# Kernel tuning notes

Measured on AMD Instinct MI355X. Metric: run time of the kernel, lower is better.

The kernel has to match this reference:

```python
import jax, jax.numpy as jnp
import numpy as np

DIM = 128
N_ITER = 8
L_SIZE = 80000
C_SIZE = 120000
N_EDGES = 480000


def _mlp(x, w1, b1, w2, b2):
    # 2-layer MLP with ReLU (satbench_n_mlp_layers=2, activation='relu')
    return jnp.maximum(x @ w1 + b1, 0.0) @ w2 + b2


def _layer_norm(x, g, b, eps=1e-5):
    mu = jnp.mean(x, axis=-1, keepdims=True)
    var = jnp.var(x, axis=-1, keepdims=True)
    return (x - mu) * jax.lax.rsqrt(var + eps) * g + b


def _ln_lstm_cell(x, h, c, wi, wh, g_ih, b_ih, g_hh, b_hh, g_c, b_c):
    # LayerNormBasicLSTMCell: LN on input/hidden gate pre-activations and on new cell state
    gates = _layer_norm(x @ wi, g_ih, b_ih) + _layer_norm(h @ wh, g_hh, b_hh)
    i, f, g, o = jnp.split(gates, 4, axis=1)
    new_c = jax.nn.sigmoid(f) * c + jax.nn.sigmoid(i) * jnp.tanh(g)
    new_h = jax.nn.sigmoid(o) * jnp.tanh(_layer_norm(new_c, g_c, b_c))
    return new_h, new_c


def setup_inputs() -> dict:
    key = jax.random.key(0)
    ks = jax.random.split(key, 24)
    d = DIM
    s1 = 1.0 / np.sqrt(d)
    s2 = 1.0 / np.sqrt(2 * d)
    inp = {
        'l_size': L_SIZE,
        'c_size': C_SIZE,
        'l_edge_index': jax.random.randint(ks[0], (N_EDGES,), 0, L_SIZE),
        'c_edge_index': jax.random.randint(ks[1], (N_EDGES,), 0, C_SIZE),
        'l_emb': jax.random.normal(ks[2], (L_SIZE, d), jnp.float32),
        'c_emb': jax.random.normal(ks[3], (C_SIZE, d), jnp.float32),
        # l2c message MLP
        'l2c_w1': jax.random.normal(ks[4], (d, d), jnp.float32) * s1,
        'l2c_b1': jnp.zeros((d,), jnp.float32),
        'l2c_w2': jax.random.normal(ks[5], (d, d), jnp.float32) * s1,
        'l2c_b2': jnp.zeros((d,), jnp.float32),
        # c2l message MLP
        'c2l_w1': jax.random.normal(ks[6], (d, d), jnp.float32) * s1,
        'c2l_b1': jnp.zeros((d,), jnp.float32),
        'c2l_w2': jax.random.normal(ks[7], (d, d), jnp.float32) * s1,
        'c2l_b2': jnp.zeros((d,), jnp.float32),
        # clause update LSTM (input=d)
        'cu_wi': jax.random.normal(ks[8], (d, 4 * d), jnp.float32) * s1,
        'cu_wh': jax.random.normal(ks[9], (d, 4 * d), jnp.float32) * s1,
        'cu_g_ih': jnp.ones((4 * d,), jnp.float32),
        'cu_b_ih': jnp.zeros((4 * d,), jnp.float32),
        'cu_g_hh': jnp.ones((4 * d,), jnp.float32),
        'cu_b_hh': jnp.zeros((4 * d,), jnp.float32),
        'cu_g_c': jnp.ones((d,), jnp.float32),
        'cu_b_c': jnp.zeros((d,), jnp.float32),
        # literal update LSTM (input=2*d)
        'lu_wi': jax.random.normal(ks[10], (2 * d, 4 * d), jnp.float32) * s2,
        'lu_wh': jax.random.normal(ks[11], (d, 4 * d), jnp.float32) * s1,
        'lu_g_ih': jnp.ones((4 * d,), jnp.float32),
        'lu_b_ih': jnp.zeros((4 * d,), jnp.float32),
        'lu_g_hh': jnp.ones((4 * d,), jnp.float32),
        'lu_b_hh': jnp.zeros((4 * d,), jnp.float32),
        'lu_g_c': jnp.ones((d,), jnp.float32),
        'lu_b_c': jnp.zeros((d,), jnp.float32),
    }
    return inp


def reference(l_size, c_size, l_edge_index, c_edge_index, l_emb, c_emb,
              l2c_w1, l2c_b1, l2c_w2, l2c_b2,
              c2l_w1, c2l_b1, c2l_w2, c2l_b2,
              cu_wi, cu_wh, cu_g_ih, cu_b_ih, cu_g_hh, cu_b_hh, cu_g_c, cu_b_c,
              lu_wi, lu_wh, lu_g_ih, lu_b_ih, lu_g_hh, lu_b_hh, lu_g_c, lu_b_c):
    d = l_emb.shape[1]
    l_state = jnp.zeros((l_size, d), l_emb.dtype)
    c_state = jnp.zeros((c_size, d), c_emb.dtype)
    l_embs = [l_emb]
    c_embs = [c_emb]
    for _ in range(N_ITER):
        # literal -> clause
        l_msg_feat = _mlp(l_emb, l2c_w1, l2c_b1, l2c_w2, l2c_b2)
        l2c_msg = l_msg_feat[l_edge_index]                             # [E, d] gather
        l2c_aggr = jax.ops.segment_sum(l2c_msg, c_edge_index, num_segments=c_size)
        c_emb, c_state = _ln_lstm_cell(l2c_aggr, c_emb, c_state,
                                       cu_wi, cu_wh, cu_g_ih, cu_b_ih,
                                       cu_g_hh, cu_b_hh, cu_g_c, cu_b_c)
        c_embs.append(c_emb)
        # clause -> literal
        c_msg_feat = _mlp(c_emb, c2l_w1, c2l_b1, c2l_w2, c2l_b2)
        c2l_msg = c_msg_feat[c_edge_index]
        c2l_aggr = jax.ops.segment_sum(c2l_msg, l_edge_index, num_segments=l_size)
        # flip pos/neg literal embeddings (l2l message)
        pl, ul = jnp.split(l_emb.reshape(l_size // 2, 2 * d), 2, axis=1)
        l2l_msg = jnp.concatenate([ul, pl], axis=1).reshape(l_size, d)
        l_emb, l_state = _ln_lstm_cell(jnp.concatenate([c2l_aggr, l2l_msg], axis=1),
                                       l_emb, l_state,
                                       lu_wi, lu_wh, lu_g_ih, lu_b_ih,
                                       lu_g_hh, lu_b_hh, lu_g_c, lu_b_c)
        l_embs.append(l_emb)
    return jnp.stack(l_embs), jnp.stack(c_embs)
```

## Files before the change

kernel.cpp:

```cpp
#include <hip/hip_runtime.h>
#include <hip/hip_bf16.h>

#define L_SIZE 80000
#define C_SIZE 120000
#define N_EDGES 480000
#define DIM 128
#define GDIM 512
#define N_ITER 8
#define MAXDEG 64

typedef __attribute__((ext_vector_type(8))) short short8;
typedef __attribute__((ext_vector_type(4))) float f32x4;

__device__ __forceinline__ ushort f2bf(float f) {
    uint u = __float_as_uint(f);
    u = u + 0x7FFFu + ((u >> 16) & 1u);
    return (ushort)(u >> 16);
}
__device__ __forceinline__ float bf2f(ushort h) {
    return __uint_as_float(((uint)h) << 16);
}
__device__ __forceinline__ void split2(float f, short& hi, short& lo) {
    uint u = __float_as_uint(f);
    hi = (short)(u >> 16);
    float r = f - __uint_as_float(u & 0xFFFF0000u);
    lo = (short)(__float_as_uint(r) >> 16);
}
__device__ __forceinline__ float sigmf(float x) { return 1.f / (1.f + __expf(-x)); }
__device__ __forceinline__ float tanh_f(float x) {
    float e = __expf(2.f * x);
    return 1.f - 2.f / (e + 1.f);
}
__device__ __forceinline__ f32x4 fzero4() {
    f32x4 v; v[0] = v[1] = v[2] = v[3] = 0.f; return v;
}

__global__ __launch_bounds__(256) void fill_ell(
    const int* __restrict__ src, const int* __restrict__ dst,
    int* __restrict__ cnt, int* __restrict__ ell)
{
    int i = blockIdx.x * 256 + threadIdx.x;
    int d = dst[i];
    int pos = atomicAdd(&cnt[d], 1);
    ell[(size_t)d * MAXDEG + pos] = src[i];
}

__global__ __launch_bounds__(256) void pack_w2(const float* __restrict__ W,
                                               ushort* __restrict__ Ph,
                                               ushort* __restrict__ Pl, int K, int N)
{
    int NC = N / 16;
    int total = K * N;
    for (int o = blockIdx.x * 256 + threadIdx.x; o < total; o += gridDim.x * 256) {
        int j = o & 7, hi = (o >> 3) & 3, c = (o >> 5) & 15;
        int rest = o >> 9;
        int cc = rest % NC, ks = rest / NC;
        int row = ks * 32 + hi * 8 + j, col = cc * 16 + c;
        float v = W[(size_t)row * N + col];
        ushort h = f2bf(v);
        Ph[o] = h;
        Pl[o] = f2bf(v - bf2f(h));
    }
}

__device__ __forceinline__ void stageA2(const float* __restrict__ src, int rowBase,
                                        ushort* dst, int tid, int nrows)
{
    const int planeB = nrows * 256;
    for (int idx = tid * 8; idx < nrows * 128; idx += 512 * 8) {
        int r = idx >> 7, k8 = idx & 127;
        const float* p = src + (size_t)(rowBase + r) * DIM + k8;
        float4 v0 = *(const float4*)p;
        float4 v1 = *(const float4*)(p + 4);
        float f[8] = {v0.x, v0.y, v0.z, v0.w, v1.x, v1.y, v1.z, v1.w};
        short8 hi8, lo8;
        #pragma unroll
        for (int j = 0; j < 8; ++j) {
            short h, l;
            split2(f[j], h, l);
            hi8[j] = h;
            lo8[j] = l;
        }
        int boff = r * 256 + ((k8 * 2) ^ ((r & 7) << 4));
        *(short8*)((char*)dst + boff) = hi8;
        *(short8*)((char*)dst + planeB + boff) = lo8;
    }
}

__device__ __forceinline__ short8 readA(const ushort* As, int mi, int k0, int lane)
{
    int r = mi * 16 + (lane & 15);
    int kb = (k0 * 2 + ((lane >> 4) << 4)) ^ ((r & 7) << 4);
    return *(const short8*)((const char*)As + r * 256 + kb);
}

__device__ __forceinline__ short8 readAf(const ushort* As, int mi, int k0, int lane)
{
    int r = (mi * 16 + (lane & 15)) ^ 1;
    int kb = (k0 * 2 + ((lane >> 4) << 4)) ^ ((r & 7) << 4);
    return *(const short8*)((const char*)As + r * 256 + kb);
}

__device__ __forceinline__ short8 readB(const ushort* P, int ks, int NC, int cc,
                                        int laneOff)
{
    return *(const short8*)((const char*)P + (((size_t)(ks * NC + cc)) << 10) + laneOff);
}

#define MFMA3(acc, ah, al, bh, bl)                                              \
    acc = __builtin_amdgcn_mfma_f32_16x16x32_bf16(ah, bh, acc, 0, 0, 0);        \
    acc = __builtin_amdgcn_mfma_f32_16x16x32_bf16(ah, bl, acc, 0, 0, 0);        \
    acc = __builtin_amdgcn_mfma_f32_16x16x32_bf16(al, bh, acc, 0, 0, 0);

__global__ __launch_bounds__(512, 4) void mlp_kernel(
    const float* __restrict__ A,
    const ushort* __restrict__ w1Ph, const ushort* __restrict__ w1Pl,
    const float* __restrict__ b1,
    const ushort* __restrict__ w2Ph, const ushort* __restrict__ w2Pl,
    const float* __restrict__ b2,
    float* __restrict__ msg)
{
    __shared__ __align__(16) ushort AsIn[2 * 64 * 128];
    __shared__ __align__(16) ushort AsHid[2 * 64 * 128];
    const int tid = threadIdx.x;
    const int wv = tid >> 6, lane = tid & 63;
    const int cl = lane & 15, hi = lane >> 4;
    const int rowBase = blockIdx.x * 64;
    const int laneOff = (cl * 4 + hi) * 16;
    const int col = wv * 16 + cl;

    stageA2(A, rowBase, AsIn, tid, 64);
    float b1c = b1[col], b2c = b2[col];
    __syncthreads();

    f32x4 acc[4];
    #pragma unroll
    for (int mi = 0; mi < 4; ++mi) acc[mi] = fzero4();
    #pragma unroll
    for (int ks = 0; ks < 4; ++ks) {
        short8 bh = readB(w1Ph, ks, 8, wv, laneOff);
        short8 bl = readB(w1Pl, ks, 8, wv, laneOff);
        #pragma unroll
        for (int mi = 0; mi < 4; ++mi) {
            short8 ah = readA(AsIn, mi, ks * 32, lane);
            short8 al = readA(AsIn + 64 * 128, mi, ks * 32, lane);
            MFMA3(acc[mi], ah, al, bh, bl);
        }
    }
    #pragma unroll
    for (int mi = 0; mi < 4; ++mi)
        #pragma unroll
        for (int q = 0; q < 4; ++q) {
            int row = mi * 16 + hi * 4 + q;
            float v = fmaxf(acc[mi][q] + b1c, 0.f);
            short h2, l2;
            split2(v, h2, l2);
            int boff = row * 256 + ((2 * col) ^ ((row & 7) << 4));
            *(short*)((char*)AsHid + boff) = h2;
            *(short*)((char*)AsHid + 64 * 256 + boff) = l2;
        }
    __syncthreads();

    f32x4 acc2[4];
    #pragma unroll
    for (int mi = 0; mi < 4; ++mi) acc2[mi] = fzero4();
    #pragma unroll
    for (int ks = 0; ks < 4; ++ks) {
        short8 bh = readB(w2Ph, ks, 8, wv, laneOff);
        short8 bl = readB(w2Pl, ks, 8, wv, laneOff);
        #pragma unroll
        for (int mi = 0; mi < 4; ++mi) {
            short8 ah = readA(AsHid, mi, ks * 32, lane);
            short8 al = readA(AsHid + 64 * 128, mi, ks * 32, lane);
            MFMA3(acc2[mi], ah, al, bh, bl);
        }
    }
    #pragma unroll
    for (int mi = 0; mi < 4; ++mi)
        #pragma unroll
        for (int q = 0; q < 4; ++q) {
            int row = mi * 16 + hi * 4 + q;
            msg[(size_t)(rowBase + row) * DIM + col] = acc2[mi][q] + b2c;
        }
}

template<int KX>
__global__ __launch_bounds__(512, 4) void lstm_kernel(
    const float* __restrict__ msg, const int* __restrict__ cnt,
    const int* __restrict__ ell,
    const float* __restrict__ Hsrc,
    const ushort* __restrict__ wiPh, const ushort* __restrict__ wiPl,
    const ushort* __restrict__ whPh, const ushort* __restrict__ whPl,
    const float* __restrict__ g_ih, const float* __restrict__ b_ih,
    const float* __restrict__ g_hh, const float* __restrict__ b_hh,
    const float* __restrict__ g_c,  const float* __restrict__ b_c,
    float* __restrict__ c_state, float* __restrict__ h_out)
{
    __shared__ __align__(16) ushort AsX0[2 * 32 * 128];
    __shared__ __align__(16) ushort AsH [2 * 32 * 128];
    __shared__ float Cs[32][132];
    __shared__ float red4f[32 * 33];
    __shared__ float lnstf[32 * 4];
    __shared__ float red2f[32 * 17];
    __shared__ float lncf[32 * 2];

    const int tid = threadIdx.x;
    const int wv = tid >> 6, lane = tid & 63;
    const int cl = lane & 15, hi = lane >> 4;
    const int rowBase = blockIdx.x * 32;
    const int laneOff = (cl * 4 + hi) * 16;
    const int d = wv * 16 + cl;

    stageA2(Hsrc, rowBase, AsH, tid, 32);
    {
        #pragma unroll
        for (int idx = tid * 4; idx < 32 * 128; idx += 512 * 4) {
            int r = idx >> 7, c = idx & 127;
            *(float4*)&Cs[r][c] =
                *(const float4*)(c_state + (size_t)(rowBase + r) * DIM + c);
        }
    }

    {
        int r = tid >> 4;
        int d8 = (tid & 15) << 3;
        int row = rowBase + r;
        int deg = cnt[row];
        const int* sl = ell + (size_t)row * MAXDEG;
        float a0=0,a1=0,a2=0,a3=0,a4=0,a5=0,a6=0,a7=0;
        for (int k = 0; k < deg; k += 4) {
            int i0 = sl[k], i1 = sl[k+1], i2 = sl[k+2], i3 = sl[k+3];
            const float* m0 = msg + (size_t)i0 * DIM + d8;
            const float* m1 = msg + (size_t)i1 * DIM + d8;
            const float* m2 = msg + (size_t)i2 * DIM + d8;
            const float* m3 = msg + (size_t)i3 * DIM + d8;
            float4 p00 = *(const float4*)m0,       p01 = *(const float4*)(m0 + 4);
            float4 p10 = *(const float4*)m1,       p11 = *(const float4*)(m1 + 4);
            float4 p20 = *(const float4*)m2,       p21 = *(const float4*)(m2 + 4);
            float4 p30 = *(const float4*)m3,       p31 = *(const float4*)(m3 + 4);
            float w1 = (k + 1 < deg) ? 1.f : 0.f;
            float w2 = (k + 2 < deg) ? 1.f : 0.f;
            float w3 = (k + 3 < deg) ? 1.f : 0.f;
            a0 += p00.x; a1 += p00.y; a2 += p00.z; a3 += p00.w;
            a4 += p01.x; a5 += p01.y; a6 += p01.z; a7 += p01.w;
            a0 += w1 * p10.x; a1 += w1 * p10.y; a2 += w1 * p10.z; a3 += w1 * p10.w;
            a4 += w1 * p11.x; a5 += w1 * p11.y; a6 += w1 * p11.z; a7 += w1 * p11.w;
            a0 += w2 * p20.x; a1 += w2 * p20.y; a2 += w2 * p20.z; a3 += w2 * p20.w;
            a4 += w2 * p21.x; a5 += w2 * p21.y; a6 += w2 * p21.z; a7 += w2 * p21.w;
            a0 += w3 * p30.x; a1 += w3 * p30.y; a2 += w3 * p30.z; a3 += w3 * p30.w;
            a4 += w3 * p31.x; a5 += w3 * p31.y; a6 += w3 * p31.z; a7 += w3 * p31.w;
        }
        float f[8] = {a0,a1,a2,a3,a4,a5,a6,a7};
        short8 hi8, lo8;
        #pragma unroll
        for (int j = 0; j < 8; ++j) {
            short h, l;
            split2(f[j], h, l);
            hi8[j] = h;
            lo8[j] = l;
        }
        int boff = r * 256 + ((d8 * 2) ^ ((r & 7) << 4));
        *(short8*)((char*)AsX0 + boff) = hi8;
        *(short8*)((char*)AsX0 + 32 * 256 + boff) = lo8;
    }

    float gih[4], bih[4], ghh[4], bhh[4];
    #pragma unroll
    for (int jb = 0; jb < 4; ++jb) {
        int col = jb * 128 + d;
        gih[jb] = g_ih[col]; bih[jb] = b_ih[col];
        ghh[jb] = g_hh[col]; bhh[jb] = b_hh[col];
    }
    const float gcv = g_c[d], bcv = b_c[d];
    __syncthreads();

    f32x4 xacc[2][4], hacc[2][4];
    #pragma unroll
    for (int mi = 0; mi < 2; ++mi)
        #pragma unroll
        for (int jb = 0; jb < 4; ++jb) { xacc[mi][jb] = fzero4(); hacc[mi][jb] = fzero4(); }

    #pragma unroll
    for (int ks = 0; ks < KX; ++ks) {
        int k0 = (ks & 3) * 32;
        short8 axh0, axl0, axh1, axl1;
        if (KX == 8 && ks >= 4) {
            axh0 = readAf(AsH, 0, k0, lane);
            axl0 = readAf(AsH + 32 * 128, 0, k0, lane);
            axh1 = readAf(AsH, 1, k0, lane);
            axl1 = readAf(AsH + 32 * 128, 1, k0, lane);
        } else {
            axh0 = readA(AsX0, 0, k0, lane);
            axl0 = readA(AsX0 + 32 * 128, 0, k0, lane);
            axh1 = readA(AsX0, 1, k0, lane);
            axl1 = readA(AsX0 + 32 * 128, 1, k0, lane);
        }
        #pragma unroll
        for (int jb = 0; jb < 4; ++jb) {
            short8 bh = readB(wiPh, ks, 32, jb * 8 + wv, laneOff);
            short8 bl = readB(wiPl, ks, 32, jb * 8 + wv, laneOff);
            MFMA3(xacc[0][jb], axh0, axl0, bh, bl);
            MFMA3(xacc[1][jb], axh1, axl1, bh, bl);
        }
        if (ks < 4) {
            short8 ahh0 = readA(AsH, 0, k0, lane);
            short8 ahl0 = readA(AsH + 32 * 128, 0, k0, lane);
            short8 ahh1 = readA(AsH, 1, k0, lane);
            short8 ahl1 = readA(AsH + 32 * 128, 1, k0, lane);
            #pragma unroll
            for (int jb = 0; jb < 4; ++jb) {
                short8 bh = readB(whPh, ks, 32, jb * 8 + wv, laneOff);
                short8 bl = readB(whPl, ks, 32, jb * 8 + wv, laneOff);
                MFMA3(hacc[0][jb], ahh0, ahl0, bh, bl);
                MFMA3(hacc[1][jb], ahh1, ahl1, bh, bl);
            }
        }
    }

    #pragma unroll
    for (int mi = 0; mi < 2; ++mi)
        #pragma unroll
        for (int q = 0; q < 4; ++q) {
            float px = 0.f, pqx = 0.f, ph = 0.f, pqh = 0.f;
            #pragma unroll
            for (int jb = 0; jb < 4; ++jb) {
                float v = xacc[mi][jb][q]; px += v; pqx += v * v;
                float u = hacc[mi][jb][q]; ph += u; pqh += u * u;
            }
            #pragma unroll
            for (int m = 1; m < 16; m <<= 1) {
                px += __shfl_xor(px, m); pqx += __shfl_xor(pqx, m);
                ph += __shfl_xor(ph, m); pqh += __shfl_xor(pqh, m);
            }
            if (cl == 0) {
                int row = mi * 16 + hi * 4 + q;
                float* rp = red4f + row * 33 + wv * 4;
                rp[0] = px; rp[1] = pqx; rp[2] = ph; rp[3] = pqh;
            }
        }
    __syncthreads();
    if (tid < 32) {
        float sx = 0.f, qx = 0.f, sh = 0.f, qh = 0.f;
        const float* rp = red4f + tid * 33;
        for (int ww = 0; ww < 8; ++ww) {
            sx += rp[ww * 4 + 0]; qx += rp[ww * 4 + 1];
            sh += rp[ww * 4 + 2]; qh += rp[ww * 4 + 3];
        }
        const float inv = 1.f / 512.f;
        float mux = sx * inv, muh = sh * inv;
        lnstf[tid * 4 + 0] = mux;
        lnstf[tid * 4 + 1] = rsqrtf(qx * inv - mux * mux + 1e-5f);
        lnstf[tid * 4 + 2] = muh;
        lnstf[tid * 4 + 3] = rsqrtf(qh * inv - muh * muh + 1e-5f);
    }
    __syncthreads();

    float cn[2][4], og[2][4];
    #pragma unroll
    for (int mi = 0; mi < 2; ++mi)
        #pragma unroll
        for (int q = 0; q < 4; ++q) {
            int row = mi * 16 + hi * 4 + q;
            float mux = lnstf[row * 4 + 0], rx = lnstf[row * 4 + 1];
            float muh = lnstf[row * 4 + 2], rh = lnstf[row * 4 + 3];
            float g4[4];
            #pragma unroll
            for (int jb = 0; jb < 4; ++jb)
                g4[jb] = (xacc[mi][jb][q] - mux) * rx * gih[jb] + bih[jb]
                       + (hacc[mi][jb][q] - muh) * rh * ghh[jb] + bhh[jb];
            float cp = Cs[row][d];
            float cv = sigmf(g4[1]) * cp + sigmf(g4[0]) * tanh_f(g4[2]);
            cn[mi][q] = cv; og[mi][q] = g4[3];
            float sc = cv, qc = cv * cv;
            #pragma unroll
            for (int m = 1; m < 16; m <<= 1) {
                sc += __shfl_xor(sc, m); qc += __shfl_xor(qc, m);
            }
            if (cl == 0) {
                float* rp = red2f + row * 17 + wv * 2;
                rp[0] = sc; rp[1] = qc;
            }
        }
    __syncthreads();
    if (tid < 32) {
        float sc = 0.f, qc = 0.f;
        const float* rp = red2f + tid * 17;
        for (int ww = 0; ww < 8; ++ww) { sc += rp[ww * 2]; qc += rp[ww * 2 + 1]; }
        const float inv = 1.f / 128.f;
        float mu = sc * inv;
        lncf[tid * 2 + 0] = mu;
        lncf[tid * 2 + 1] = rsqrtf(qc * inv - mu * mu + 1e-5f);
    }
    __syncthreads();

    #pragma unroll
    for (int mi = 0; mi < 2; ++mi)
        #pragma unroll
        for (int q = 0; q < 4; ++q) {
            int row = mi * 16 + hi * 4 + q;
            size_t go = (size_t)(rowBase + row) * DIM + d;
            float cv = cn[mi][q];
            float hv = sigmf(og[mi][q]) *
                       tanh_f((cv - lncf[row * 2]) * lncf[row * 2 + 1] * gcv + bcv);
            c_state[go] = cv;
            h_out[go] = hv;
        }
}

extern "C" void kernel_launch(void* const* d_in, const int* in_sizes, int n_in,
                              void* d_out, int out_size, void* d_ws, size_t ws_size,
                              hipStream_t stream)
{
    const int*   l_edge  = (const int*)d_in[2];
    const int*   c_edge  = (const int*)d_in[3];
    const float* l_emb0  = (const float*)d_in[4];
    const float* c_emb0  = (const float*)d_in[5];
    const float* l2c_w1  = (const float*)d_in[6];
    const float* l2c_b1  = (const float*)d_in[7];
    const float* l2c_w2  = (const float*)d_in[8];
    const float* l2c_b2  = (const float*)d_in[9];
    const float* c2l_w1  = (const float*)d_in[10];
    const float* c2l_b1  = (const float*)d_in[11];
    const float* c2l_w2  = (const float*)d_in[12];
    const float* c2l_b2  = (const float*)d_in[13];
    const float* cu_wi   = (const float*)d_in[14];
    const float* cu_wh   = (const float*)d_in[15];
    const float* cu_g_ih = (const float*)d_in[16];
    const float* cu_b_ih = (const float*)d_in[17];
    const float* cu_g_hh = (const float*)d_in[18];
    const float* cu_b_hh = (const float*)d_in[19];
    const float* cu_g_c  = (const float*)d_in[20];
    const float* cu_b_c  = (const float*)d_in[21];
    const float* lu_wi   = (const float*)d_in[22];
    const float* lu_wh   = (const float*)d_in[23];
    const float* lu_g_ih = (const float*)d_in[24];
    const float* lu_b_ih = (const float*)d_in[25];
    const float* lu_g_hh = (const float*)d_in[26];
    const float* lu_b_hh = (const float*)d_in[27];
    const float* lu_g_c  = (const float*)d_in[28];
    const float* lu_b_c  = (const float*)d_in[29];

    float* out = (float*)d_out;
    float* l_slab = out;
    float* c_slab = out + (size_t)9 * L_SIZE * DIM;

    char* wp = (char*)d_ws;
    float*  l_state = (float*)wp;  wp += (size_t)L_SIZE * DIM * 4;
    float*  c_state = (float*)wp;  wp += (size_t)C_SIZE * DIM * 4;
    float*  msg     = (float*)wp;  wp += (size_t)C_SIZE * DIM * 4;
    int* c_cnt = (int*)wp; wp += C_SIZE * 4;
    int* l_cnt = (int*)wp; wp += L_SIZE * 4;
    int* c_ell = (int*)wp; wp += (size_t)C_SIZE * MAXDEG * 4;
    int* l_ell = (int*)wp; wp += (size_t)L_SIZE * MAXDEG * 4;
    ushort* l2c_w1Ph = (ushort*)wp; wp += 128 * 128 * 2;
    ushort* l2c_w1Pl = (ushort*)wp; wp += 128 * 128 * 2;
    ushort* l2c_w2Ph = (ushort*)wp; wp += 128 * 128 * 2;
    ushort* l2c_w2Pl = (ushort*)wp; wp += 128 * 128 * 2;
    ushort* c2l_w1Ph = (ushort*)wp; wp += 128 * 128 * 2;
    ushort* c2l_w1Pl = (ushort*)wp; wp += 128 * 128 * 2;
    ushort* c2l_w2Ph = (ushort*)wp; wp += 128 * 128 * 2;
    ushort* c2l_w2Pl = (ushort*)wp; wp += 128 * 128 * 2;
    ushort* cu_wiPh  = (ushort*)wp; wp += 128 * 512 * 2;
    ushort* cu_wiPl  = (ushort*)wp; wp += 128 * 512 * 2;
    ushort* cu_whPh  = (ushort*)wp; wp += 128 * 512 * 2;
    ushort* cu_whPl  = (ushort*)wp; wp += 128 * 512 * 2;
    ushort* lu_wiPh  = (ushort*)wp; wp += 256 * 512 * 2;
    ushort* lu_wiPl  = (ushort*)wp; wp += 256 * 512 * 2;
    ushort* lu_whPh  = (ushort*)wp; wp += 128 * 512 * 2;
    ushort* lu_whPl  = (ushort*)wp; wp += 128 * 512 * 2;

    const int eb = N_EDGES / 256;

    hipMemsetAsync(c_cnt, 0, C_SIZE * 4, stream);
    hipMemsetAsync(l_cnt, 0, L_SIZE * 4, stream);
    hipMemsetAsync(c_ell, 0, (size_t)C_SIZE * MAXDEG * 4, stream);
    hipMemsetAsync(l_ell, 0, (size_t)L_SIZE * MAXDEG * 4, stream);
    fill_ell<<<eb, 256, 0, stream>>>(l_edge, c_edge, c_cnt, c_ell);
    fill_ell<<<eb, 256, 0, stream>>>(c_edge, l_edge, l_cnt, l_ell);

    pack_w2<<<64, 256, 0, stream>>>(l2c_w1, l2c_w1Ph, l2c_w1Pl, 128, 128);
    pack_w2<<<64, 256, 0, stream>>>(l2c_w2, l2c_w2Ph, l2c_w2Pl, 128, 128);
    pack_w2<<<64, 256, 0, stream>>>(c2l_w1, c2l_w1Ph, c2l_w1Pl, 128, 128);
    pack_w2<<<64, 256, 0, stream>>>(c2l_w2, c2l_w2Ph, c2l_w2Pl, 128, 128);
    pack_w2<<<256, 256, 0, stream>>>(cu_wi, cu_wiPh, cu_wiPl, 128, 512);
    pack_w2<<<256, 256, 0, stream>>>(cu_wh, cu_whPh, cu_whPl, 128, 512);
    pack_w2<<<512, 256, 0, stream>>>(lu_wi, lu_wiPh, lu_wiPl, 256, 512);
    pack_w2<<<256, 256, 0, stream>>>(lu_wh, lu_whPh, lu_whPl, 128, 512);

    hipMemcpyAsync(l_slab, l_emb0, (size_t)L_SIZE * DIM * sizeof(float),
                   hipMemcpyDeviceToDevice, stream);
    hipMemcpyAsync(c_slab, c_emb0, (size_t)C_SIZE * DIM * sizeof(float),
                   hipMemcpyDeviceToDevice, stream);
    hipMemsetAsync(l_state, 0, (size_t)L_SIZE * DIM * sizeof(float), stream);
    hipMemsetAsync(c_state, 0, (size_t)C_SIZE * DIM * sizeof(float), stream);

    for (int t = 0; t < N_ITER; ++t) {
        const float* le = l_slab + (size_t)t * L_SIZE * DIM;
        const float* ce = c_slab + (size_t)t * C_SIZE * DIM;
        float* le1 = l_slab + (size_t)(t + 1) * L_SIZE * DIM;
        float* ce1 = c_slab + (size_t)(t + 1) * C_SIZE * DIM;

        mlp_kernel<<<L_SIZE / 64, 512, 0, stream>>>(le, l2c_w1Ph, l2c_w1Pl, l2c_b1,
                                                    l2c_w2Ph, l2c_w2Pl, l2c_b2, msg);
        lstm_kernel<4><<<C_SIZE / 32, 512, 0, stream>>>(
            msg, c_cnt, c_ell, ce,
            cu_wiPh, cu_wiPl, cu_whPh, cu_whPl,
            cu_g_ih, cu_b_ih, cu_g_hh, cu_b_hh, cu_g_c, cu_b_c,
            c_state, ce1);

        mlp_kernel<<<C_SIZE / 64, 512, 0, stream>>>(ce1, c2l_w1Ph, c2l_w1Pl, c2l_b1,
                                                    c2l_w2Ph, c2l_w2Pl, c2l_b2, msg);
        lstm_kernel<8><<<L_SIZE / 32, 512, 0, stream>>>(
            msg, l_cnt, l_ell, le,
            lu_wiPh, lu_wiPl, lu_whPh, lu_whPl,
            lu_g_ih, lu_b_ih, lu_g_hh, lu_b_hh, lu_g_c, lu_b_c,
            l_state, le1);
    }
}
```

Measured before the change: 5.372 ms.

## Fuse message MLPs into LSTM epilogues and stage messages in output slab

Each LSTM kernel now runs the next stage's 2-layer message MLP on its freshly computed hidden rows. It splits them into bf16 hi/lo in shared memory and writes the messages directly, which removes both standalone MLP launches per iteration and the re-read of embeddings from global memory. The literal-to-clause messages are placed in the next output slab slot, which is overwritten only after the clause LSTM has consumed them, so one MLP launch before the loop seeds the first iteration. The shared-memory staging of the previous cell state is also dropped in favour of direct global reads, which lowers LDS use. In exchange, each LSTM block takes on extra MFMA work and two more barriers.

```diff
diff --git a/kernel.cpp b/kernel.cpp
--- a/kernel.cpp
+++ b/kernel.cpp
@@ -194,11 +194,15 @@
     const float* __restrict__ g_ih, const float* __restrict__ b_ih,
     const float* __restrict__ g_hh, const float* __restrict__ b_hh,
     const float* __restrict__ g_c,  const float* __restrict__ b_c,
-    float* __restrict__ c_state, float* __restrict__ h_out)
+    float* __restrict__ c_state, float* __restrict__ h_out,
+    const ushort* __restrict__ m1Ph, const ushort* __restrict__ m1Pl,
+    const float* __restrict__ mb1,
+    const ushort* __restrict__ m2Ph, const ushort* __restrict__ m2Pl,
+    const float* __restrict__ mb2,
+    float* __restrict__ msg_out)
 {
     __shared__ __align__(16) ushort AsX0[2 * 32 * 128];
     __shared__ __align__(16) ushort AsH [2 * 32 * 128];
-    __shared__ float Cs[32][132];
     __shared__ float red4f[32 * 33];
     __shared__ float lnstf[32 * 4];
     __shared__ float red2f[32 * 17];
@@ -212,14 +216,6 @@
     const int d = wv * 16 + cl;
 
     stageA2(Hsrc, rowBase, AsH, tid, 32);
-    {
-        #pragma unroll
-        for (int idx = tid * 4; idx < 32 * 128; idx += 512 * 4) {
-            int r = idx >> 7, c = idx & 127;
-            *(float4*)&Cs[r][c] =
-                *(const float4*)(c_state + (size_t)(rowBase + r) * DIM + c);
-        }
-    }
 
     {
         int r = tid >> 4;
@@ -368,7 +364,7 @@
             for (int jb = 0; jb < 4; ++jb)
                 g4[jb] = (xacc[mi][jb][q] - mux) * rx * gih[jb] + bih[jb]
                        + (hacc[mi][jb][q] - muh) * rh * ghh[jb] + bhh[jb];
-            float cp = Cs[row][d];
+            float cp = c_state[(size_t)(rowBase + row) * DIM + d];
             float cv = sigmf(g4[1]) * cp + sigmf(g4[0]) * tanh_f(g4[2]);
             cn[mi][q] = cv; og[mi][q] = g4[3];
             float sc = cv, qc = cv * cv;
@@ -404,7 +400,65 @@
                        tanh_f((cv - lncf[row * 2]) * lncf[row * 2 + 1] * gcv + bcv);
             c_state[go] = cv;
             h_out[go] = hv;
-        }
+            if (msg_out) {
+                short h2, l2;
+                split2(hv, h2, l2);
+                int boff = row * 256 + ((2 * d) ^ ((row & 7) << 4));
+                *(short*)((char*)AsX0 + boff) = h2;
+                *(short*)((char*)AsX0 + 32 * 256 + boff) = l2;
+            }
+        }
+
+    if (msg_out) {
+        float mb1c = mb1[d], mb2c = mb2[d];
+        __syncthreads();
+        f32x4 macc[2];
+        macc[0] = fzero4(); macc[1] = fzero4();
+        #pragma unroll
+        for (int ks = 0; ks < 4; ++ks) {
+            short8 bh = readB(m1Ph, ks, 8, wv, laneOff);
+            short8 bl = readB(m1Pl, ks, 8, wv, laneOff);
+            #pragma unroll
+            for (int mi = 0; mi < 2; ++mi) {
+                short8 ah = readA(AsX0, mi, ks * 32, lane);
+                short8 al = readA(AsX0 + 32 * 128, mi, ks * 32, lane);
+                MFMA3(macc[mi], ah, al, bh, bl);
+            }
+        }
+        #pragma unroll
+        for (int mi = 0; mi < 2; ++mi)
+            #pragma unroll
+            for (int q = 0; q < 4; ++q) {
+                int row = mi * 16 + hi * 4 + q;
+                float v = fmaxf(macc[mi][q] + mb1c, 0.f);
+                short h2, l2;
+                split2(v, h2, l2);
+                int boff = row * 256 + ((2 * d) ^ ((row & 7) << 4));
+                *(short*)((char*)AsH + boff) = h2;
+                *(short*)((char*)AsH + 32 * 256 + boff) = l2;
+            }
+        __syncthreads();
+        f32x4 macc2[2];
+        macc2[0] = fzero4(); macc2[1] = fzero4();
+        #pragma unroll
+        for (int ks = 0; ks < 4; ++ks) {
+            short8 bh = readB(m2Ph, ks, 8, wv, laneOff);
+            short8 bl = readB(m2Pl, ks, 8, wv, laneOff);
+            #pragma unroll
+            for (int mi = 0; mi < 2; ++mi) {
+                short8 ah = readA(AsH, mi, ks * 32, lane);
+                short8 al = readA(AsH + 32 * 128, mi, ks * 32, lane);
+                MFMA3(macc2[mi], ah, al, bh, bl);
+            }
+        }
+        #pragma unroll
+        for (int mi = 0; mi < 2; ++mi)
+            #pragma unroll
+            for (int q = 0; q < 4; ++q) {
+                int row = mi * 16 + hi * 4 + q;
+                msg_out[(size_t)(rowBase + row) * DIM + d] = macc2[mi][q] + mb2c;
+            }
+    }
 }
 
 extern "C" void kernel_launch(void* const* d_in, const int* in_sizes, int n_in,
@@ -447,7 +501,7 @@
     char* wp = (char*)d_ws;
     float*  l_state = (float*)wp;  wp += (size_t)L_SIZE * DIM * 4;
     float*  c_state = (float*)wp;  wp += (size_t)C_SIZE * DIM * 4;
-    float*  msg     = (float*)wp;  wp += (size_t)C_SIZE * DIM * 4;
+    float*  msgC    = (float*)wp;  wp += (size_t)C_SIZE * DIM * 4;
     int* c_cnt = (int*)wp; wp += C_SIZE * 4;
     int* l_cnt = (int*)wp; wp += L_SIZE * 4;
     int* c_ell = (int*)wp; wp += (size_t)C_SIZE * MAXDEG * 4;
@@ -494,26 +548,31 @@
     hipMemsetAsync(l_state, 0, (size_t)L_SIZE * DIM * sizeof(float), stream);
     hipMemsetAsync(c_state, 0, (size_t)C_SIZE * DIM * sizeof(float), stream);
 
+    mlp_kernel<<<L_SIZE / 64, 512, 0, stream>>>(
+        l_slab, l2c_w1Ph, l2c_w1Pl, l2c_b1, l2c_w2Ph, l2c_w2Pl, l2c_b2,
+        l_slab + (size_t)L_SIZE * DIM);
+
     for (int t = 0; t < N_ITER; ++t) {
         const float* le = l_slab + (size_t)t * L_SIZE * DIM;
         const float* ce = c_slab + (size_t)t * C_SIZE * DIM;
         float* le1 = l_slab + (size_t)(t + 1) * L_SIZE * DIM;
         float* ce1 = c_slab + (size_t)(t + 1) * C_SIZE * DIM;
-
-        mlp_kernel<<<L_SIZE / 64, 512, 0, stream>>>(le, l2c_w1Ph, l2c_w1Pl, l2c_b1,
-                                                    l2c_w2Ph, l2c_w2Pl, l2c_b2, msg);
+        float* msgL   = l_slab + (size_t)(t + 1) * L_SIZE * DIM;
+        float* msgLn  = (t + 2 <= 8) ? l_slab + (size_t)(t + 2) * L_SIZE * DIM
+                                     : nullptr;
+
         lstm_kernel<4><<<C_SIZE / 32, 512, 0, stream>>>(
-            msg, c_cnt, c_ell, ce,
+            msgL, c_cnt, c_ell, ce,
             cu_wiPh, cu_wiPl, cu_whPh, cu_whPl,
             cu_g_ih, cu_b_ih, cu_g_hh, cu_b_hh, cu_g_c, cu_b_c,
-            c_state, ce1);
-
-        mlp_kernel<<<C_SIZE / 64, 512, 0, stream>>>(ce1, c2l_w1Ph, c2l_w1Pl, c2l_b1,
-                                                    c2l_w2Ph, c2l_w2Pl, c2l_b2, msg);
+            c_state, ce1,
+            c2l_w1Ph, c2l_w1Pl, c2l_b1, c2l_w2Ph, c2l_w2Pl, c2l_b2, msgC);
+
         lstm_kernel<8><<<L_SIZE / 32, 512, 0, stream>>>(
-            msg, l_cnt, l_ell, le,
+            msgC, l_cnt, l_ell, le,
             lu_wiPh, lu_wiPl, lu_whPh, lu_whPl,
             lu_g_ih, lu_b_ih, lu_g_hh, lu_b_hh, lu_g_c, lu_b_c,
-            l_state, le1);
-    }
-}
+            l_state, le1,
+            l2c_w1Ph, l2c_w1Pl, l2c_b1, l2c_w2Ph, l2c_w2Pl, l2c_b2, msgLn);
+    }
+}
```

Result: slower. 5.679 ms (+5.7%).

## Halve rows per block in MLP and LSTM kernels to raise occupancy

Applied to the files above, without the earlier changes.

The MLP kernel now processes 32 rows per block instead of 64, and the LSTM kernel processes 16 instead of 32. Launch bounds move from 4 to 6 blocks per CU, the grids double, and the LSTM no longer stages the cell state in LDS, reading it directly from global memory. The intent is to cut registers and LDS per block so more blocks fit on each CU and latency hiding improves. In exchange, each block reuses the packed weight fragments over fewer rows, so weight traffic per row roughly doubles, and barrier overhead per row goes up.

```diff
diff --git a/kernel.cpp b/kernel.cpp
--- a/kernel.cpp
+++ b/kernel.cpp
@@ -10,6 +10,7 @@
 #define MAXDEG 64
 
 typedef __attribute__((ext_vector_type(8))) short short8;
+typedef __attribute__((ext_vector_type(4))) short short4v;
 typedef __attribute__((ext_vector_type(4))) float f32x4;
 
 __device__ __forceinline__ ushort f2bf(float f) {
@@ -112,7 +113,7 @@
     acc = __builtin_amdgcn_mfma_f32_16x16x32_bf16(ah, bl, acc, 0, 0, 0);        \
     acc = __builtin_amdgcn_mfma_f32_16x16x32_bf16(al, bh, acc, 0, 0, 0);
 
-__global__ __launch_bounds__(512, 4) void mlp_kernel(
+__global__ __launch_bounds__(512, 6) void mlp_kernel(
     const float* __restrict__ A,
     const ushort* __restrict__ w1Ph, const ushort* __restrict__ w1Pl,
     const float* __restrict__ b1,
@@ -120,35 +121,34 @@
     const float* __restrict__ b2,
     float* __restrict__ msg)
 {
-    __shared__ __align__(16) ushort AsIn[2 * 64 * 128];
-    __shared__ __align__(16) ushort AsHid[2 * 64 * 128];
+    __shared__ __align__(16) ushort AsIn[2 * 32 * 128];
+    __shared__ __align__(16) ushort AsHid[2 * 32 * 128];
     const int tid = threadIdx.x;
     const int wv = tid >> 6, lane = tid & 63;
     const int cl = lane & 15, hi = lane >> 4;
-    const int rowBase = blockIdx.x * 64;
+    const int rowBase = blockIdx.x * 32;
     const int laneOff = (cl * 4 + hi) * 16;
     const int col = wv * 16 + cl;
 
-    stageA2(A, rowBase, AsIn, tid, 64);
-    float b1c = b1[col], b2c = b2[col];
-    __syncthreads();
-
-    f32x4 acc[4];
-    #pragma unroll
-    for (int mi = 0; mi < 4; ++mi) acc[mi] = fzero4();
+    stageA2(A, rowBase, AsIn, tid, 32);
+    __syncthreads();
+
+    f32x4 acc[2];
+    acc[0] = fzero4(); acc[1] = fzero4();
     #pragma unroll
     for (int ks = 0; ks < 4; ++ks) {
         short8 bh = readB(w1Ph, ks, 8, wv, laneOff);
         short8 bl = readB(w1Pl, ks, 8, wv, laneOff);
         #pragma unroll
-        for (int mi = 0; mi < 4; ++mi) {
+        for (int mi = 0; mi < 2; ++mi) {
             short8 ah = readA(AsIn, mi, ks * 32, lane);
-            short8 al = readA(AsIn + 64 * 128, mi, ks * 32, lane);
+            short8 al = readA(AsIn + 32 * 128, mi, ks * 32, lane);
             MFMA3(acc[mi], ah, al, bh, bl);
         }
     }
-    #pragma unroll
-    for (int mi = 0; mi < 4; ++mi)
+    float b1c = b1[col];
+    #pragma unroll
+    for (int mi = 0; mi < 2; ++mi)
         #pragma unroll
         for (int q = 0; q < 4; ++q) {
             int row = mi * 16 + hi * 4 + q;
@@ -157,26 +157,26 @@
             split2(v, h2, l2);
             int boff = row * 256 + ((2 * col) ^ ((row & 7) << 4));
             *(short*)((char*)AsHid + boff) = h2;
-            *(short*)((char*)AsHid + 64 * 256 + boff) = l2;
-        }
-    __syncthreads();
-
-    f32x4 acc2[4];
-    #pragma unroll
-    for (int mi = 0; mi < 4; ++mi) acc2[mi] = fzero4();
+            *(short*)((char*)AsHid + 32 * 256 + boff) = l2;
+        }
+    __syncthreads();
+
+    f32x4 acc2[2];
+    acc2[0] = fzero4(); acc2[1] = fzero4();
     #pragma unroll
     for (int ks = 0; ks < 4; ++ks) {
         short8 bh = readB(w2Ph, ks, 8, wv, laneOff);
         short8 bl = readB(w2Pl, ks, 8, wv, laneOff);
         #pragma unroll
-        for (int mi = 0; mi < 4; ++mi) {
+        for (int mi = 0; mi < 2; ++mi) {
             short8 ah = readA(AsHid, mi, ks * 32, lane);
-            short8 al = readA(AsHid + 64 * 128, mi, ks * 32, lane);
+            short8 al = readA(AsHid + 32 * 128, mi, ks * 32, lane);
             MFMA3(acc2[mi], ah, al, bh, bl);
         }
     }
-    #pragma unroll
-    for (int mi = 0; mi < 4; ++mi)
+    float b2c = b2[col];
+    #pragma unroll
+    for (int mi = 0; mi < 2; ++mi)
         #pragma unroll
         for (int q = 0; q < 4; ++q) {
             int row = mi * 16 + hi * 4 + q;
@@ -185,7 +185,7 @@
 }
 
 template<int KX>
-__global__ __launch_bounds__(512, 4) void lstm_kernel(
+__global__ __launch_bounds__(512, 6) void lstm_kernel(
     const float* __restrict__ msg, const int* __restrict__ cnt,
     const int* __restrict__ ell,
     const float* __restrict__ Hsrc,
@@ -196,150 +196,112 @@
     const float* __restrict__ g_c,  const float* __restrict__ b_c,
     float* __restrict__ c_state, float* __restrict__ h_out)
 {
-    __shared__ __align__(16) ushort AsX0[2 * 32 * 128];
-    __shared__ __align__(16) ushort AsH [2 * 32 * 128];
-    __shared__ float Cs[32][132];
-    __shared__ float red4f[32 * 33];
-    __shared__ float lnstf[32 * 4];
-    __shared__ float red2f[32 * 17];
-    __shared__ float lncf[32 * 2];
+    __shared__ __align__(16) ushort AsX0[2 * 16 * 128];
+    __shared__ __align__(16) ushort AsH [2 * 16 * 128];
+    __shared__ float red4f[16 * 33];
+    __shared__ float lnstf[16 * 4];
+    __shared__ float red2f[16 * 17];
+    __shared__ float lncf[16 * 2];
 
     const int tid = threadIdx.x;
     const int wv = tid >> 6, lane = tid & 63;
     const int cl = lane & 15, hi = lane >> 4;
-    const int rowBase = blockIdx.x * 32;
+    const int rowBase = blockIdx.x * 16;
     const int laneOff = (cl * 4 + hi) * 16;
     const int d = wv * 16 + cl;
 
-    stageA2(Hsrc, rowBase, AsH, tid, 32);
+    stageA2(Hsrc, rowBase, AsH, tid, 16);
+
     {
-        #pragma unroll
-        for (int idx = tid * 4; idx < 32 * 128; idx += 512 * 4) {
-            int r = idx >> 7, c = idx & 127;
-            *(float4*)&Cs[r][c] =
-                *(const float4*)(c_state + (size_t)(rowBase + r) * DIM + c);
-        }
-    }
-
-    {
-        int r = tid >> 4;
-        int d8 = (tid & 15) << 3;
+        int r = tid >> 5;
+        int d4 = (tid & 31) << 2;
         int row = rowBase + r;
         int deg = cnt[row];
         const int* sl = ell + (size_t)row * MAXDEG;
-        float a0=0,a1=0,a2=0,a3=0,a4=0,a5=0,a6=0,a7=0;
+        float a0 = 0.f, a1 = 0.f, a2 = 0.f, a3 = 0.f;
         for (int k = 0; k < deg; k += 4) {
             int i0 = sl[k], i1 = sl[k+1], i2 = sl[k+2], i3 = sl[k+3];
-            const float* m0 = msg + (size_t)i0 * DIM + d8;
-            const float* m1 = msg + (size_t)i1 * DIM + d8;
-            const float* m2 = msg + (size_t)i2 * DIM + d8;
-            const float* m3 = msg + (size_t)i3 * DIM + d8;
-            float4 p00 = *(const float4*)m0,       p01 = *(const float4*)(m0 + 4);
-            float4 p10 = *(const float4*)m1,       p11 = *(const float4*)(m1 + 4);
-            float4 p20 = *(const float4*)m2,       p21 = *(const float4*)(m2 + 4);
-            float4 p30 = *(const float4*)m3,       p31 = *(const float4*)(m3 + 4);
+            float4 p0 = *(const float4*)(msg + (size_t)i0 * DIM + d4);
+            float4 p1 = *(const float4*)(msg + (size_t)i1 * DIM + d4);
+            float4 p2 = *(const float4*)(msg + (size_t)i2 * DIM + d4);
+            float4 p3 = *(const float4*)(msg + (size_t)i3 * DIM + d4);
             float w1 = (k + 1 < deg) ? 1.f : 0.f;
             float w2 = (k + 2 < deg) ? 1.f : 0.f;
             float w3 = (k + 3 < deg) ? 1.f : 0.f;
-            a0 += p00.x; a1 += p00.y; a2 += p00.z; a3 += p00.w;
-            a4 += p01.x; a5 += p01.y; a6 += p01.z; a7 += p01.w;
-            a0 += w1 * p10.x; a1 += w1 * p10.y; a2 += w1 * p10.z; a3 += w1 * p10.w;
-            a4 += w1 * p11.x; a5 += w1 * p11.y; a6 += w1 * p11.z; a7 += w1 * p11.w;
-            a0 += w2 * p20.x; a1 += w2 * p20.y; a2 += w2 * p20.z; a3 += w2 * p20.w;
-            a4 += w2 * p21.x; a5 += w2 * p21.y; a6 += w2 * p21.z; a7 += w2 * p21.w;
-            a0 += w3 * p30.x; a1 += w3 * p30.y; a2 += w3 * p30.z; a3 += w3 * p30.w;
-            a4 += w3 * p31.x; a5 += w3 * p31.y; a6 += w3 * p31.z; a7 += w3 * p31.w;
-        }
-        float f[8] = {a0,a1,a2,a3,a4,a5,a6,a7};
-        short8 hi8, lo8;
-        #pragma unroll
-        for (int j = 0; j < 8; ++j) {
+            a0 += p0.x;      a1 += p0.y;      a2 += p0.z;      a3 += p0.w;
+            a0 += w1 * p1.x; a1 += w1 * p1.y; a2 += w1 * p1.z; a3 += w1 * p1.w;
+            a0 += w2 * p2.x; a1 += w2 * p2.y; a2 += w2 * p2.z; a3 += w2 * p2.w;
+            a0 += w3 * p3.x; a1 += w3 * p3.y; a2 += w3 * p3.z; a3 += w3 * p3.w;
+        }
+        float f[4] = {a0, a1, a2, a3};
+        short4v hi4, lo4;
+        #pragma unroll
+        for (int j = 0; j < 4; ++j) {
             short h, l;
             split2(f[j], h, l);
-            hi8[j] = h;
-            lo8[j] = l;
-        }
-        int boff = r * 256 + ((d8 * 2) ^ ((r & 7) << 4));
-        *(short8*)((char*)AsX0 + boff) = hi8;
-        *(short8*)((char*)AsX0 + 32 * 256 + boff) = lo8;
-    }
-
-    float gih[4], bih[4], ghh[4], bhh[4];
-    #pragma unroll
-    for (int jb = 0; jb < 4; ++jb) {
-        int col = jb * 128 + d;
-        gih[jb] = g_ih[col]; bih[jb] = b_ih[col];
-        ghh[jb] = g_hh[col]; bhh[jb] = b_hh[col];
-    }
-    const float gcv = g_c[d], bcv = b_c[d];
-    __syncthreads();
-
-    f32x4 xacc[2][4], hacc[2][4];
-    #pragma unroll
-    for (int mi = 0; mi < 2; ++mi)
-        #pragma unroll
-        for (int jb = 0; jb < 4; ++jb) { xacc[mi][jb] = fzero4(); hacc[mi][jb] = fzero4(); }
+            hi4[j] = h;
+            lo4[j] = l;
+        }
+        int boff = r * 256 + ((d4 * 2) ^ ((r & 7) << 4));
+        *(short4v*)((char*)AsX0 + boff) = hi4;
+        *(short4v*)((char*)AsX0 + 16 * 256 + boff) = lo4;
+    }
+    __syncthreads();
+
+    f32x4 xacc[4], hacc[4];
+    #pragma unroll
+    for (int jb = 0; jb < 4; ++jb) { xacc[jb] = fzero4(); hacc[jb] = fzero4(); }
 
     #pragma unroll
     for (int ks = 0; ks < KX; ++ks) {
         int k0 = (ks & 3) * 32;
-        short8 axh0, axl0, axh1, axl1;
+        short8 axh, axl;
         if (KX == 8 && ks >= 4) {
-            axh0 = readAf(AsH, 0, k0, lane);
-            axl0 = readAf(AsH + 32 * 128, 0, k0, lane);
-            axh1 = readAf(AsH, 1, k0, lane);
-            axl1 = readAf(AsH + 32 * 128, 1, k0, lane);
+            axh = readAf(AsH, 0, k0, lane);
+            axl = readAf(AsH + 16 * 128, 0, k0, lane);
         } else {
-            axh0 = readA(AsX0, 0, k0, lane);
-            axl0 = readA(AsX0 + 32 * 128, 0, k0, lane);
-            axh1 = readA(AsX0, 1, k0, lane);
-            axl1 = readA(AsX0 + 32 * 128, 1, k0, lane);
+            axh = readA(AsX0, 0, k0, lane);
+            axl = readA(AsX0 + 16 * 128, 0, k0, lane);
         }
         #pragma unroll
         for (int jb = 0; jb < 4; ++jb) {
             short8 bh = readB(wiPh, ks, 32, jb * 8 + wv, laneOff);
             short8 bl = readB(wiPl, ks, 32, jb * 8 + wv, laneOff);
-            MFMA3(xacc[0][jb], axh0, axl0, bh, bl);
-            MFMA3(xacc[1][jb], axh1, axl1, bh, bl);
+            MFMA3(xacc[jb], axh, axl, bh, bl);
         }
         if (ks < 4) {
-            short8 ahh0 = readA(AsH, 0, k0, lane);
-            short8 ahl0 = readA(AsH + 32 * 128, 0, k0, lane);
-            short8 ahh1 = readA(AsH, 1, k0, lane);
-            short8 ahl1 = readA(AsH + 32 * 128, 1, k0, lane);
+            short8 ahh = readA(AsH, 0, k0, lane);
+            short8 ahl = readA(AsH + 16 * 128, 0, k0, lane);
             #pragma unroll
             for (int jb = 0; jb < 4; ++jb) {
                 short8 bh = readB(whPh, ks, 32, jb * 8 + wv, laneOff);
                 short8 bl = readB(whPl, ks, 32, jb * 8 + wv, laneOff);
-                MFMA3(hacc[0][jb], ahh0, ahl0, bh, bl);
-                MFMA3(hacc[1][jb], ahh1, ahl1, bh, bl);
+                MFMA3(hacc[jb], ahh, ahl, bh, bl);
             }
         }
     }
 
     #pragma unroll
-    for (int mi = 0; mi < 2; ++mi)
-        #pragma unroll
-        for (int q = 0; q < 4; ++q) {
-            float px = 0.f, pqx = 0.f, ph = 0.f, pqh = 0.f;
-            #pragma unroll
-            for (int jb = 0; jb < 4; ++jb) {
-                float v = xacc[mi][jb][q]; px += v; pqx += v * v;
-                float u = hacc[mi][jb][q]; ph += u; pqh += u * u;
-            }
-            #pragma unroll
-            for (int m = 1; m < 16; m <<= 1) {
-                px += __shfl_xor(px, m); pqx += __shfl_xor(pqx, m);
-                ph += __shfl_xor(ph, m); pqh += __shfl_xor(pqh, m);
-            }
-            if (cl == 0) {
-                int row = mi * 16 + hi * 4 + q;
-                float* rp = red4f + row * 33 + wv * 4;
-                rp[0] = px; rp[1] = pqx; rp[2] = ph; rp[3] = pqh;
-            }
-        }
-    __syncthreads();
-    if (tid < 32) {
+    for (int q = 0; q < 4; ++q) {
+        float px = 0.f, pqx = 0.f, ph = 0.f, pqh = 0.f;
+        #pragma unroll
+        for (int jb = 0; jb < 4; ++jb) {
+            float v = xacc[jb][q]; px += v; pqx += v * v;
+            float u = hacc[jb][q]; ph += u; pqh += u * u;
+        }
+        #pragma unroll
+        for (int m = 1; m < 16; m <<= 1) {
+            px += __shfl_xor(px, m); pqx += __shfl_xor(pqx, m);
+            ph += __shfl_xor(ph, m); pqh += __shfl_xor(pqh, m);
+        }
+        if (cl == 0) {
+            int row = hi * 4 + q;
+            float* rp = red4f + row * 33 + wv * 4;
+            rp[0] = px; rp[1] = pqx; rp[2] = ph; rp[3] = pqh;
+        }
+    }
+    __syncthreads();
+    if (tid < 16) {
         float sx = 0.f, qx = 0.f, sh = 0.f, qh = 0.f;
         const float* rp = red4f + tid * 33;
         for (int ww = 0; ww < 8; ++ww) {
@@ -355,34 +317,40 @@
     }
     __syncthreads();
 
-    float cn[2][4], og[2][4];
-    #pragma unroll
-    for (int mi = 0; mi < 2; ++mi)
-        #pragma unroll
-        for (int q = 0; q < 4; ++q) {
-            int row = mi * 16 + hi * 4 + q;
-            float mux = lnstf[row * 4 + 0], rx = lnstf[row * 4 + 1];
-            float muh = lnstf[row * 4 + 2], rh = lnstf[row * 4 + 3];
-            float g4[4];
-            #pragma unroll
-            for (int jb = 0; jb < 4; ++jb)
-                g4[jb] = (xacc[mi][jb][q] - mux) * rx * gih[jb] + bih[jb]
-                       + (hacc[mi][jb][q] - muh) * rh * ghh[jb] + bhh[jb];
-            float cp = Cs[row][d];
-            float cv = sigmf(g4[1]) * cp + sigmf(g4[0]) * tanh_f(g4[2]);
-            cn[mi][q] = cv; og[mi][q] = g4[3];
-            float sc = cv, qc = cv * cv;
-            #pragma unroll
-            for (int m = 1; m < 16; m <<= 1) {
-                sc += __shfl_xor(sc, m); qc += __shfl_xor(qc, m);
-            }
-            if (cl == 0) {
-                float* rp = red2f + row * 17 + wv * 2;
-                rp[0] = sc; rp[1] = qc;
-            }
-        }
-    __syncthreads();
-    if (tid < 32) {
+    float gih[4], bih[4], ghh[4], bhh[4];
+    #pragma unroll
+    for (int jb = 0; jb < 4; ++jb) {
+        int col = jb * 128 + d;
+        gih[jb] = g_ih[col]; bih[jb] = b_ih[col];
+        ghh[jb] = g_hh[col]; bhh[jb] = b_hh[col];
+    }
+
+    float cn[4], og[4];
+    #pragma unroll
+    for (int q = 0; q < 4; ++q) {
+        int row = hi * 4 + q;
+        float mux = lnstf[row * 4 + 0], rx = lnstf[row * 4 + 1];
+        float muh = lnstf[row * 4 + 2], rh = lnstf[row * 4 + 3];
+        float g4[4];
+        #pragma unroll
+        for (int jb = 0; jb < 4; ++jb)
+            g4[jb] = (xacc[jb][q] - mux) * rx * gih[jb] + bih[jb]
+                   + (hacc[jb][q] - muh) * rh * ghh[jb] + bhh[jb];
+        float cp = c_state[(size_t)(rowBase + row) * DIM + d];
+        float cv = sigmf(g4[1]) * cp + sigmf(g4[0]) * tanh_f(g4[2]);
+        cn[q] = cv; og[q] = g4[3];
+        float sc = cv, qc = cv * cv;
+        #pragma unroll
+        for (int m = 1; m < 16; m <<= 1) {
+            sc += __shfl_xor(sc, m); qc += __shfl_xor(qc, m);
+        }
+        if (cl == 0) {
+            float* rp = red2f + row * 17 + wv * 2;
+            rp[0] = sc; rp[1] = qc;
+        }
+    }
+    __syncthreads();
+    if (tid < 16) {
         float sc = 0.f, qc = 0.f;
         const float* rp = red2f + tid * 17;
         for (int ww = 0; ww < 8; ++ww) { sc += rp[ww * 2]; qc += rp[ww * 2 + 1]; }
@@ -393,18 +361,17 @@
     }
     __syncthreads();
 
-    #pragma unroll
-    for (int mi = 0; mi < 2; ++mi)
-        #pragma unroll
-        for (int q = 0; q < 4; ++q) {
-            int row = mi * 16 + hi * 4 + q;
-            size_t go = (size_t)(rowBase + row) * DIM + d;
-            float cv = cn[mi][q];
-            float hv = sigmf(og[mi][q]) *
-                       tanh_f((cv - lncf[row * 2]) * lncf[row * 2 + 1] * gcv + bcv);
-            c_state[go] = cv;
-            h_out[go] = hv;
-        }
+    const float gcv = g_c[d], bcv = b_c[d];
+    #pragma unroll
+    for (int q = 0; q < 4; ++q) {
+        int row = hi * 4 + q;
+        size_t go = (size_t)(rowBase + row) * DIM + d;
+        float cv = cn[q];
+        float hv = sigmf(og[q]) *
+                   tanh_f((cv - lncf[row * 2]) * lncf[row * 2 + 1] * gcv + bcv);
+        c_state[go] = cv;
+        h_out[go] = hv;
+    }
 }
 
 extern "C" void kernel_launch(void* const* d_in, const int* in_sizes, int n_in,
@@ -500,17 +467,17 @@
         float* le1 = l_slab + (size_t)(t + 1) * L_SIZE * DIM;
         float* ce1 = c_slab + (size_t)(t + 1) * C_SIZE * DIM;
 
-        mlp_kernel<<<L_SIZE / 64, 512, 0, stream>>>(le, l2c_w1Ph, l2c_w1Pl, l2c_b1,
+        mlp_kernel<<<L_SIZE / 32, 512, 0, stream>>>(le, l2c_w1Ph, l2c_w1Pl, l2c_b1,
                                                     l2c_w2Ph, l2c_w2Pl, l2c_b2, msg);
-        lstm_kernel<4><<<C_SIZE / 32, 512, 0, stream>>>(
+        lstm_kernel<4><<<C_SIZE / 16, 512, 0, stream>>>(
             msg, c_cnt, c_ell, ce,
             cu_wiPh, cu_wiPl, cu_whPh, cu_whPl,
             cu_g_ih, cu_b_ih, cu_g_hh, cu_b_hh, cu_g_c, cu_b_c,
             c_state, ce1);
 
-        mlp_kernel<<<C_SIZE / 64, 512, 0, stream>>>(ce1, c2l_w1Ph, c2l_w1Pl, c2l_b1,
+        mlp_kernel<<<C_SIZE / 32, 512, 0, stream>>>(ce1, c2l_w1Ph, c2l_w1Pl, c2l_b1,
                                                     c2l_w2Ph, c2l_w2Pl, c2l_b2, msg);
-        lstm_kernel<8><<<L_SIZE / 32, 512, 0, stream>>>(
+        lstm_kernel<8><<<L_SIZE / 16, 512, 0, stream>>>(
             msg, l_cnt, l_ell, le,
             lu_wiPh, lu_wiPl, lu_whPh, lu_whPl,
             lu_g_ih, lu_b_ih, lu_g_hh, lu_b_hh, lu_g_c, lu_b_c,
```

After: 5.974 ms. +11.2%, slower.
